# Optimization experiments

Hardware: AMD Instinct MI355X
Metric: run time of the kernel (lower is better)

## Reference

```python
import jax, jax.numpy as jnp
import numpy as np

N_BALLS, BALL, DIM, HEADS = 16, 512, 256, 8
DH = DIM // HEADS            # 32
WIN = BALL // 16             # sliding window = 32
CBS = BALL // 16             # compress block size = 32
CST = BALL // 32             # compress stride = 16
FBS = BALL // 16             # fine (selection) block size = 32
NCB = (BALL - CBS) // CST + 1  # 31 compressed blocks
NFB = BALL // FBS              # 16 fine blocks
NB = BALL // WIN               # 16 sliding blocks
SCALE = DH ** -0.5

# ---- static index maps / masks (numpy, baked at trace time) ----
_qi = np.arange(BALL)
WIDX = np.arange(NCB)[:, None] * CST + np.arange(CBS)[None, :]          # (NCB, CBS)
_blk_end = np.arange(NCB) * CST + CBS - 1
CMASK = np.concatenate([np.ones((BALL, 1), bool), _qi[:, None] >= _blk_end[None, :]], axis=1)  # (m, NCB+1), col0 = mem kv
OVERLAP = np.zeros((NCB, NFB), np.float32)  # fraction of compressed block j overlapping fine block f
for _j in range(NCB):
    _a, _b = _j * CST, _j * CST + CBS
    for _f in range(NFB):
        _fa, _fb = _f * FBS, (_f + 1) * FBS
        OVERLAP[_j, _f] = max(0, min(_b, _fb) - max(_a, _fa)) / CBS
SELMASK = np.arange(NFB)[None, :] < (_qi // FBS)[:, None]   # only strictly-past fine blocks selectable
HAS_SEL = (_qi // FBS) > 0
OWN_TRI = (_qi % FBS)[:, None] >= np.arange(FBS)[None, :]   # causal mask inside own fine block
_qq = np.arange(WIN)[None, :, None]
_kk = np.arange(2 * WIN)[None, None, :]
_bb = np.arange(NB)[:, None, None]
SWMASK = (_kk > _qq) & (_kk <= _qq + WIN) & ((_bb > 0) | (_kk >= WIN))
NEG = -jnp.inf


def _rot(x, tpos):
    # interleaved rotary over full head dim; x: (n,H,m,DH)
    d2 = DH // 2
    inv = 1.0 / (10000.0 ** (jnp.arange(d2, dtype=jnp.float32) / d2))
    ang = tpos[:, None] * inv[None, :]
    cos, sin = jnp.cos(ang), jnp.sin(ang)
    x1, x2 = x[..., 0::2], x[..., 1::2]
    return jnp.stack((x1 * cos - x2 * sin, x1 * sin + x2 * cos), axis=-1).reshape(x.shape)


def _gmlp(xw, w1, w2):
    # per-head grouped MLP compressing each window: (n,H,NCB,CBS,DH) -> (n,H,NCB,DH)
    f = xw.reshape(xw.shape[0], HEADS, NCB, CBS * DH)
    h = jax.nn.relu(jnp.einsum('nhbi,hio->nhbo', f, w1))
    return jnp.einsum('nhbi,hio->nhbo', h, w2)


def _forward(x, pos, Wpe, bpe, rms_w, Wqkv, kpos, vpos, kw1, kw2, vw1, vw2, mem_ck, mem_cv, Wg, Wo):
    n, m = N_BALLS, BALL
    # relative position embedding w.r.t. ball center (eq. 9)
    pb = pos.reshape(n, m, -1)
    rel = pb - pb.mean(axis=1, keepdims=True)
    hx = x.reshape(n, m, DIM) + rel @ Wpe + bpe
    # RMSNorm
    hn = hx * jax.lax.rsqrt(jnp.mean(hx * hx, axis=-1, keepdims=True) + 1e-6) * rms_w
    q, k, v = jnp.split(hn @ Wqkv, 3, axis=-1)
    heads = lambda t: t.reshape(n, m, HEADS, DH).transpose(0, 2, 1, 3)
    q, k, v = heads(q), heads(k), heads(v)
    tpos = jnp.arange(m, dtype=jnp.float32)
    rq, rk = _rot(q, tpos), _rot(k, tpos)

    # ---- compressed branch (non-rotated q/k, intra-block pos emb, 1 learned mem kv) ----
    kw = k[:, :, WIDX] + kpos[None, :, None]        # (n,H,NCB,CBS,DH)
    vw = v[:, :, WIDX] + vpos[None, :, None]
    ck = _gmlp(kw, kw1, kw2)
    cv = _gmlp(vw, vw1, vw2)
    ckf = jnp.concatenate([jnp.broadcast_to(mem_ck[None], (n, HEADS, 1, DH)), ck], axis=2)
    cvf = jnp.concatenate([jnp.broadcast_to(mem_cv[None], (n, HEADS, 1, DH)), cv], axis=2)
    csim = jnp.einsum('nhid,nhjd->nhij', q, ckf) * SCALE
    cattn = jax.nn.softmax(jnp.where(CMASK[None, None], csim, NEG), axis=-1)
    c_out = jnp.einsum('nhij,nhjd->nhid', cattn, cvf)

    # ---- fine selection: importance from compressed attn probs -> top-1 past fine block ----
    imp = jnp.einsum('nhij,jf->nhif', cattn[..., 1:], jnp.asarray(OVERLAP))  # (n,H,m,NFB)
    sel = jnp.argmax(jnp.where(SELMASK[None, None], imp, NEG), axis=-1)     # (n,H,m)
    kb = rk.reshape(n, HEADS, NFB, FBS, DH)
    vb = v.reshape(n, HEADS, NFB, FBS, DH)
    qb = rq.reshape(n, HEADS, NFB, FBS, DH)
    own_s = (jnp.einsum('nhfqd,nhfkd->nhfqk', qb, kb) * SCALE).reshape(n, HEADS, m, FBS)
    fk = jnp.take_along_axis(kb, sel[..., None, None], axis=2)  # (n,H,m,FBS,DH) gather
    fv = jnp.take_along_axis(vb, sel[..., None, None], axis=2)
    sel_s = jnp.einsum('nhid,nhikd->nhik', rq, fk) * SCALE
    scores = jnp.concatenate([jnp.where(OWN_TRI[None, None], own_s, NEG),
                              jnp.where(HAS_SEL[None, None, :, None], sel_s, NEG)], axis=-1)
    fattn = jax.nn.softmax(scores, axis=-1)
    f_out = (jnp.einsum('nhfqk,nhfkd->nhfqd', fattn[..., :FBS].reshape(n, HEADS, NFB, FBS, FBS), vb).reshape(n, HEADS, m, DH)
             + jnp.einsum('nhik,nhikd->nhid', fattn[..., FBS:], fv))

    # ---- sliding window branch (causal local attention, look-back 1 block) ----
    qw = rq.reshape(n, HEADS, NB, WIN, DH)
    kwb = rk.reshape(n, HEADS, NB, WIN, DH)
    vwb = v.reshape(n, HEADS, NB, WIN, DH)
    pad = ((0, 0), (0, 0), (1, 0), (0, 0), (0, 0))
    K2 = jnp.concatenate([jnp.pad(kwb, pad)[:, :, :NB], kwb], axis=3)
    V2 = jnp.concatenate([jnp.pad(vwb, pad)[:, :, :NB], vwb], axis=3)
    s_sw = jnp.einsum('nhbqd,nhbkd->nhbqk', qw, K2) * SCALE
    sattn = jax.nn.softmax(jnp.where(SWMASK[None, None], s_sw, NEG), axis=-1)
    sw_out = jnp.einsum('nhbqk,nhbkd->nhbqd', sattn, V2).reshape(n, HEADS, m, DH)

    # ---- sigmoid-gated combine of the 3 strategies, merge heads, out proj ----
    gates = jax.nn.sigmoid(hn @ Wg).reshape(n, m, HEADS, 3).transpose(0, 2, 1, 3)  # (n,H,m,3)
    o = c_out * gates[..., 0:1] + f_out * gates[..., 1:2] + sw_out * gates[..., 2:3]
    o = o.transpose(0, 2, 1, 3).reshape(n, m, DIM)
    return (o @ Wo).reshape(n * m, DIM)


def setup_inputs() -> dict:
    key = jax.random.key(0)
    ks = jax.random.split(key, 16)
    s = 0.02
    N = N_BALLS * BALL
    return dict(
        x=jax.random.normal(ks[0], (N, DIM), jnp.float32),
        pos=jax.random.normal(ks[1], (N, 3), jnp.float32),
        Wpe=s * jax.random.normal(ks[2], (3, DIM), jnp.float32),
        bpe=jnp.zeros((DIM,), jnp.float32),
        rms_w=jnp.ones((DIM,), jnp.float32),
        Wqkv=s * jax.random.normal(ks[3], (DIM, 3 * DIM), jnp.float32),
        kpos=s * jax.random.normal(ks[4], (HEADS, CBS, DH), jnp.float32),
        vpos=s * jax.random.normal(ks[5], (HEADS, CBS, DH), jnp.float32),
        kw1=s * jax.random.normal(ks[6], (HEADS, CBS * DH, CBS * DH), jnp.float32),
        kw2=s * jax.random.normal(ks[7], (HEADS, CBS * DH, DH), jnp.float32),
        vw1=s * jax.random.normal(ks[8], (HEADS, CBS * DH, CBS * DH), jnp.float32),
        vw2=s * jax.random.normal(ks[9], (HEADS, CBS * DH, DH), jnp.float32),
        mem_ck=s * jax.random.normal(ks[10], (HEADS, 1, DH), jnp.float32),
        mem_cv=s * jax.random.normal(ks[11], (HEADS, 1, DH), jnp.float32),
        Wg=s * jax.random.normal(ks[12], (DIM, 3 * HEADS), jnp.float32),
        Wo=s * jax.random.normal(ks[13], (DIM, DIM), jnp.float32),
    )


def reference(x, pos, Wpe, bpe, rms_w, Wqkv, kpos, vpos, kw1, kw2, vw1, vw2, mem_ck, mem_cv, Wg, Wo):
    return _forward(x, pos, Wpe, bpe, rms_w, Wqkv, kpos, vpos, kw1, kw2, vw1, vw2, mem_ck, mem_cv, Wg, Wo)
```

## Files before the change

### kernel.cpp

```cpp
#include <hip/hip_runtime.h>
#include <hip/hip_bf16.h>
#include <math.h>

#define SCALE_ 0.17677669529663687f

__global__ __launch_bounds__(256) void d_rope(float* __restrict__ rope) {
  int i = blockIdx.x * 256 + threadIdx.x;
  int t = i >> 4, j = i & 15;
  float inv = powf(10000.f, -(float)j / 16.f);
  float ang = (float)t * inv;
  rope[2 * i]     = cosf(ang);
  rope[2 * i + 1] = sinf(ang);
}

__global__ __launch_bounds__(256) void k_pm(const float* __restrict__ pos,
                                            float* __restrict__ pm) {
  __shared__ float ps[1536];
  int ball = blockIdx.x;
  for (int i = threadIdx.x; i < 1536; i += 256) ps[i] = pos[(size_t)ball * 1536 + i];
  __syncthreads();
  if (threadIdx.x < 3) {
    int c = threadIdx.x;
    float s = 0.f;
    for (int t = 0; t < 512; ++t) s += ps[t * 3 + c];
    pm[ball * 3 + c] = s * (1.f / 512.f);
  }
}

__global__ __launch_bounds__(256) void k_hn(const float* __restrict__ x,
                                            const float* __restrict__ pos,
                                            const float* __restrict__ pm,
                                            const float* __restrict__ Wpe,
                                            const float* __restrict__ bpe,
                                            const float* __restrict__ rmsw,
                                            const float* __restrict__ Wg,
                                            float* __restrict__ hn,
                                            float* __restrict__ gates) {
  __shared__ float hx[32][257];
  __shared__ float rr[32][3];
  __shared__ float invs[32];
  int tb = blockIdx.x * 32;
  if (threadIdx.x < 96) {
    int tok = threadIdx.x / 3, c = threadIdx.x % 3;
    rr[tok][c] = pos[(size_t)(tb + tok) * 3 + c] - pm[((tb + tok) >> 9) * 3 + c];
  }
  __syncthreads();
  for (int i = threadIdx.x; i < 8192; i += 256) {
    int tok = i >> 8, d = i & 255;
    float h = x[(size_t)(tb + tok) * 256 + d] + rr[tok][0] * Wpe[d] + rr[tok][1] * Wpe[256 + d]
            + rr[tok][2] * Wpe[512 + d] + bpe[d];
    hx[tok][d] = h;
  }
  __syncthreads();
  if (threadIdx.x < 32) {
    int tok = threadIdx.x;
    float ss = 0.f;
    for (int d = 0; d < 256; ++d) { float h = hx[tok][d]; ss += h * h; }
    invs[tok] = 1.f / sqrtf(ss * (1.f / 256.f) + 1e-6f);
  }
  __syncthreads();
  for (int i = threadIdx.x; i < 8192; i += 256) {
    int tok = i >> 8, d = i & 255;
    float hv = hx[tok][d] * invs[tok] * rmsw[d];
    hn[(size_t)(tb + tok) * 256 + d] = hv;
    hx[tok][d] = hv;
  }
  __syncthreads();
  for (int g = threadIdx.x; g < 768; g += 256) {
    int tok = g / 24, j = g % 24;
    float s = 0.f;
    for (int d = 0; d < 256; ++d) s += hx[tok][d] * Wg[d * 24 + j];
    gates[(size_t)(tb + tok) * 24 + j] = 1.f / (1.f + expf(-s));
  }
}

__global__ __launch_bounds__(256) void k_qkv(const float* __restrict__ A,
                                             const float* __restrict__ B,
                                             const float* __restrict__ rope,
                                             float* __restrict__ qo,
                                             float* __restrict__ ko,
                                             float* __restrict__ vo,
                                             float* __restrict__ rqo,
                                             float* __restrict__ rko) {
  __shared__ float As[32][66];
  __shared__ __align__(16) float Bs[32][68];
  const int bid = blockIdx.x;
  const int xcd = bid & 7;
  const int idx = bid >> 3;
  const int m0 = (xcd * 16 + (idx & 15)) * 64;
  const int n0 = (idx >> 4) * 64;
  const int tid = threadIdx.x;
  const int tx = tid & 15, ty = tid >> 4;
  float acc[4][4] = {};
  for (int k0 = 0; k0 < 256; k0 += 32) {
#pragma unroll
    for (int i = 0; i < 8; ++i) {
      int li = tid + i * 256;
      int mm = li >> 5, c = li & 31;
      As[c][mm] = A[(size_t)(m0 + mm) * 256 + k0 + c];
    }
#pragma unroll
    for (int i = 0; i < 8; ++i) {
      int li = tid + i * 256;
      int r = li >> 6, c = li & 63;
      Bs[r][c] = B[(size_t)(k0 + r) * 768 + n0 + c];
    }
    __syncthreads();
#pragma unroll
    for (int kk = 0; kk < 32; ++kk) {
      float2 a0 = *reinterpret_cast<const float2*>(&As[kk][ty * 4]);
      float2 a1 = *reinterpret_cast<const float2*>(&As[kk][ty * 4 + 2]);
      float4 b4 = *reinterpret_cast<const float4*>(&Bs[kk][tx * 4]);
      float a[4] = {a0.x, a0.y, a1.x, a1.y};
      float b[4] = {b4.x, b4.y, b4.z, b4.w};
#pragma unroll
      for (int i = 0; i < 4; ++i)
#pragma unroll
        for (int j = 0; j < 4; ++j) acc[i][j] += a[i] * b[j];
    }
    __syncthreads();
  }
#pragma unroll
  for (int i = 0; i < 4; ++i) {
    int row = m0 + ty * 4 + i;
    int nb = row >> 9, t = row & 511;
#pragma unroll
    for (int j = 0; j < 4; j += 2) {
      int col = n0 + tx * 4 + j;
      int which = col >> 8, cj = col & 255;
      int h = cj >> 5, d = cj & 31;
      float v1 = acc[i][j], v2 = acc[i][j + 1];
      size_t base = ((size_t)(nb * 8 + h) * 512 + t) * 32 + d;
      if (which == 0) {
        qo[base] = v1; qo[base + 1] = v2;
        int p = d >> 1;
        float cc = rope[(t * 16 + p) * 2], ss = rope[(t * 16 + p) * 2 + 1];
        rqo[base] = v1 * cc - v2 * ss; rqo[base + 1] = v1 * ss + v2 * cc;
      } else if (which == 1) {
        ko[base] = v1; ko[base + 1] = v2;
        int p = d >> 1;
        float cc = rope[(t * 16 + p) * 2], ss = rope[(t * 16 + p) * 2 + 1];
        rko[base] = v1 * cc - v2 * ss; rko[base + 1] = v1 * ss + v2 * cc;
      } else {
        vo[base] = v1; vo[base + 1] = v2;
      }
    }
  }
}

__global__ __launch_bounds__(256) void k_gmlp1(const float* __restrict__ kv,
                                               const float* __restrict__ posw,
                                               const float* __restrict__ w1,
                                               float* __restrict__ hb) {
  __shared__ float As[32][66];
  __shared__ __align__(16) float Bs[32][68];
  __shared__ int rowbase[64];
  const int bid = blockIdx.x;
  const int xcd = bid & 7;
  const int idx = bid >> 3;
  const int mt  = idx & 7;
  const int nh  = xcd * 16 + (idx >> 3);
  const int n0 = (nh & 15) * 64;
  const int h  = nh >> 4;
  const int m0 = mt * 64;
  const int tid = threadIdx.x;
  const int tx = tid & 15, ty = tid >> 4;
  if (tid < 64) {
    int row = m0 + tid;
    if (row < 496) {
      int nb = row / 31, bb = row % 31;
      rowbase[tid] = ((nb * 8 + h) * 512 + bb * 16) * 32;
    } else rowbase[tid] = -1;
  }
  __syncthreads();
  float acc[4][4] = {};
  const float* pw = posw + h * 1024;
  for (int k0 = 0; k0 < 1024; k0 += 32) {
#pragma unroll
    for (int i = 0; i < 8; ++i) {
      int li = tid + i * 256;
      int mm = li >> 5, c = li & 31;
      int base = rowbase[mm];
      float vv = 0.f;
      if (base >= 0) vv = kv[(size_t)base + k0 + c] + pw[k0 + c];
      As[c][mm] = vv;
    }
#pragma unroll
    for (int i = 0; i < 8; ++i) {
      int li = tid + i * 256;
      int r = li >> 6, c = li & 63;
      Bs[r][c] = w1[(size_t)h * 1048576 + (size_t)(k0 + r) * 1024 + n0 + c];
    }
    __syncthreads();
#pragma unroll
    for (int kk = 0; kk < 32; ++kk) {
      float2 a0 = *reinterpret_cast<const float2*>(&As[kk][ty * 4]);
      float2 a1 = *reinterpret_cast<const float2*>(&As[kk][ty * 4 + 2]);
      float4 b4 = *reinterpret_cast<const float4*>(&Bs[kk][tx * 4]);
      float a[4] = {a0.x, a0.y, a1.x, a1.y};
      float b[4] = {b4.x, b4.y, b4.z, b4.w};
#pragma unroll
      for (int i = 0; i < 4; ++i)
#pragma unroll
        for (int j = 0; j < 4; ++j) acc[i][j] += a[i] * b[j];
    }
    __syncthreads();
  }
#pragma unroll
  for (int i = 0; i < 4; ++i) {
    int row = m0 + ty * 4 + i;
    if (row < 496) {
#pragma unroll
      for (int j = 0; j < 4; ++j)
        hb[((size_t)h * 496 + row) * 1024 + n0 + tx * 4 + j] = fmaxf(acc[i][j], 0.f);
    }
  }
}

__global__ __launch_bounds__(256) void d_g2(const float* __restrict__ hh,
                                            const float* __restrict__ w2,
                                            float* __restrict__ outp) {
  int gid = blockIdx.x * 256 + threadIdx.x;
  int o = gid & 31;
  int rem = gid >> 5;
  int h = rem / 496, row = rem % 496;
  int nb = row / 31, bb = row % 31;
  const float* hr = hh + (size_t)rem * 1024;
  const float* w2p = w2 + (size_t)h * 32768 + o;
  float s = 0.f;
  for (int i = 0; i < 1024; ++i) s += hr[i] * w2p[(size_t)i * 32];
  outp[((size_t)(nb * 8 + h) * 31 + bb) * 32 + o] = s;
}

__global__ __launch_bounds__(256) void k_cattn(const float* __restrict__ q,
                                               const float* __restrict__ ck,
                                               const float* __restrict__ cv,
                                               const float* __restrict__ mem_ck,
                                               const float* __restrict__ mem_cv,
                                               const float* __restrict__ gates,
                                               float* __restrict__ obuf,
                                               int* __restrict__ sel) {
  int nh = blockIdx.x;
  int h = nh & 7, ball = nh >> 3;
  __shared__ float kf[32][33], vf[32][33];
  for (int i = threadIdx.x; i < 1024; i += 256) {
    int j = i >> 5, d = i & 31;
    kf[j][d] = (j == 0) ? mem_ck[h * 32 + d] : ck[((size_t)nh * 31 + j - 1) * 32 + d];
    vf[j][d] = (j == 0) ? mem_cv[h * 32 + d] : cv[((size_t)nh * 31 + j - 1) * 32 + d];
  }
  __syncthreads();
  for (int t = threadIdx.x; t < 512; t += 256) {
    const float* qp = q + ((size_t)nh * 512 + t) * 32;
    float qr[32];
#pragma unroll
    for (int d = 0; d < 32; ++d) qr[d] = qp[d];
    float sc[32];
    float mx = -INFINITY;
#pragma unroll
    for (int j = 0; j < 32; ++j) {
      float s = -INFINITY;
      bool valid = (j == 0) || (t >= (j - 1) * 16 + 31);
      if (valid) {
        s = 0.f;
        for (int d = 0; d < 32; ++d) s += qr[d] * kf[j][d];
        s *= SCALE_;
      }
      sc[j] = s;
      mx = fmaxf(mx, s);
    }
    float e[32];
    float den = 0.f;
#pragma unroll
    for (int j = 0; j < 32; ++j) { e[j] = expf(sc[j] - mx); den += e[j]; }
    float num[32];
#pragma unroll
    for (int d = 0; d < 32; ++d) num[d] = 0.f;
#pragma unroll
    for (int j = 0; j < 32; ++j) {
      float p = e[j];
      for (int d = 0; d < 32; ++d) num[d] += p * vf[j][d];
    }
    float inv = 1.f / den;
    float g0 = gates[(size_t)(ball * 512 + t) * 24 + h * 3];
    float* op = obuf + (size_t)(ball * 512 + t) * 256 + h * 32;
    for (int d = 0; d < 32; ++d) op[d] = num[d] * inv * g0;

    int s_idx = 0;
    if (t >= 32) {
      int fn = t >> 5;
      float best = -INFINITY;
      for (int f = 0; f < fn; ++f) {
        float im = 0.f;
#pragma unroll
        for (int j = 0; j < 31; ++j) {
          int a = j * 16, b2 = a + 32, fa = f * 32, fb = fa + 32;
          int lo = a > fa ? a : fa;
          int hi = b2 < fb ? b2 : fb;
          if (hi > lo) im += e[j + 1] * (float)(hi - lo) * (1.f / 32.f);
        }
        if (im > best) { best = im; s_idx = f; }
      }
    }
    sel[(size_t)nh * 512 + t] = s_idx;
  }
}

__global__ __launch_bounds__(256) void k_fattn(const float* __restrict__ rq,
                                               const float* __restrict__ rk,
                                               const float* __restrict__ v,
                                               const int* __restrict__ sel,
                                               const float* __restrict__ gates,
                                               float* __restrict__ obuf) {
  int f0 = blockIdx.x, h = blockIdx.y, nb = blockIdx.z;
  int nh = nb * 8 + h;
  __shared__ float rqs[32][33], rks[32][33], vs[32][33];
  for (int i = threadIdx.x; i < 1024; i += 256) {
    int r = i >> 5, d = i & 31;
    size_t base = ((size_t)nh * 512 + f0 * 32 + r) * 32 + d;
    rqs[r][d] = rq[base];
    rks[r][d] = rk[base];
    vs[r][d]  = v[base];
  }
  __syncthreads();
  int qi = threadIdx.x >> 3, l = threadIdx.x & 7;
  int t = f0 * 32 + qi;
  int sb = sel[(size_t)nh * 512 + t];
  bool hs = (t >= 32);
  float p[8];
  float mx = -INFINITY;
#pragma unroll
  for (int kk2 = 0; kk2 < 8; ++kk2) {
    int kk = l * 8 + kk2;
    float s = -INFINITY;
    if (kk < 32) {
      if (qi >= kk) {
        s = 0.f;
#pragma unroll
        for (int d = 0; d < 32; ++d) s += rqs[qi][d] * rks[kk][d];
        s *= SCALE_;
      }
    } else if (hs) {
      const float* kp = rk + ((size_t)nh * 512 + sb * 32 + (kk - 32)) * 32;
      s = 0.f;
#pragma unroll
      for (int d = 0; d < 32; ++d) s += rqs[qi][d] * kp[d];
      s *= SCALE_;
    }
    p[kk2] = s;
    mx = fmaxf(mx, s);
  }
#pragma unroll
  for (int off = 4; off; off >>= 1) mx = fmaxf(mx, __shfl_xor(mx, off, 8));
  float sum = 0.f;
#pragma unroll
  for (int kk2 = 0; kk2 < 8; ++kk2) { p[kk2] = expf(p[kk2] - mx); sum += p[kk2]; }
#pragma unroll
  for (int off = 4; off; off >>= 1) sum += __shfl_xor(sum, off, 8);
  float inv = 1.f / sum;
  float acc[32];
#pragma unroll
  for (int d = 0; d < 32; ++d) acc[d] = 0.f;
#pragma unroll
  for (int kk2 = 0; kk2 < 8; ++kk2) {
    int kk = l * 8 + kk2;
    float pw = p[kk2] * inv;
    if (kk < 32) {
#pragma unroll
      for (int d = 0; d < 32; ++d) acc[d] += pw * vs[kk][d];
    } else if (hs) {
      const float* vp = v + ((size_t)nh * 512 + sb * 32 + (kk - 32)) * 32;
#pragma unroll
      for (int d = 0; d < 32; ++d) acc[d] += pw * vp[d];
    }
  }
#pragma unroll
  for (int off = 4; off; off >>= 1) {
#pragma unroll
    for (int d = 0; d < 32; ++d) acc[d] += __shfl_xor(acc[d], off, 8);
  }
  float g1 = gates[(size_t)(nb * 512 + t) * 24 + h * 3 + 1];
  float* op = obuf + (size_t)(nb * 512 + t) * 256 + h * 32;
#pragma unroll
  for (int j = 0; j < 4; ++j) op[l * 4 + j] += acc[l * 4 + j] * g1;
}

__global__ __launch_bounds__(256) void k_swattn(const float* __restrict__ rq,
                                                const float* __restrict__ rk,
                                                const float* __restrict__ v,
                                                const float* __restrict__ gates,
                                                float* __restrict__ obuf) {
  int b = blockIdx.x, h = blockIdx.y, nb = blockIdx.z;
  int nh = nb * 8 + h;
  __shared__ float rqs[32][33], k2s[64][33], v2s[64][33];
  for (int i = threadIdx.x; i < 1024; i += 256) {
    int r = i >> 5, d = i & 31;
    rqs[r][d] = rq[((size_t)nh * 512 + b * 32 + r) * 32 + d];
  }
  for (int i = threadIdx.x; i < 2048; i += 256) {
    int r = i >> 5, d = i & 31;
    int tk = (b - 1) * 32 + r;
    float kk_ = 0.f, vv_ = 0.f;
    if (tk >= 0) {
      kk_ = rk[((size_t)nh * 512 + tk) * 32 + d];
      vv_ = v[((size_t)nh * 512 + tk) * 32 + d];
    }
    k2s[r][d] = kk_;
    v2s[r][d] = vv_;
  }
  __syncthreads();
  int qi = threadIdx.x >> 3, l = threadIdx.x & 7;
  int t = b * 32 + qi;
  float p[8];
  float mx = -INFINITY;
#pragma unroll
  for (int kk2 = 0; kk2 < 8; ++kk2) {
    int kk = l * 8 + kk2;
    bool valid = (kk > qi) && (kk <= qi + 32) && ((b > 0) || (kk >= 32));
    float s = -INFINITY;
    if (valid) {
      s = 0.f;
#pragma unroll
      for (int d = 0; d < 32; ++d) s += rqs[qi][d] * k2s[kk][d];
      s *= SCALE_;
    }
    p[kk2] = s;
    mx = fmaxf(mx, s);
  }
#pragma unroll
  for (int off = 4; off; off >>= 1) mx = fmaxf(mx, __shfl_xor(mx, off, 8));
  float sum = 0.f;
#pragma unroll
  for (int kk2 = 0; kk2 < 8; ++kk2) { p[kk2] = expf(p[kk2] - mx); sum += p[kk2]; }
#pragma unroll
  for (int off = 4; off; off >>= 1) sum += __shfl_xor(sum, off, 8);
  float inv = 1.f / sum;
  float acc[32];
#pragma unroll
  for (int d = 0; d < 32; ++d) acc[d] = 0.f;
#pragma unroll
  for (int kk2 = 0; kk2 < 8; ++kk2) {
    int kk = l * 8 + kk2;
    float pw = p[kk2] * inv;
#pragma unroll
    for (int d = 0; d < 32; ++d) acc[d] += pw * v2s[kk][d];
  }
#pragma unroll
  for (int off = 4; off; off >>= 1) {
#pragma unroll
    for (int d = 0; d < 32; ++d) acc[d] += __shfl_xor(acc[d], off, 8);
  }
  float g2 = gates[(size_t)(nb * 512 + t) * 24 + h * 3 + 2];
  float* op = obuf + (size_t)(nb * 512 + t) * 256 + h * 32;
#pragma unroll
  for (int j = 0; j < 4; ++j) op[l * 4 + j] += acc[l * 4 + j] * g2;
}

__global__ __launch_bounds__(256) void k_out(const float* __restrict__ A,
                                             const float* __restrict__ B,
                                             float* __restrict__ C) {
  __shared__ float As[32][66];
  __shared__ __align__(16) float Bs[32][68];
  const int bid = blockIdx.x;
  const int xcd = bid & 7;
  const int idx = bid >> 3;
  const int m0 = (xcd * 16 + (idx & 15)) * 64;
  const int n0 = (idx >> 4) * 64;
  const int tid = threadIdx.x;
  const int tx = tid & 15, ty = tid >> 4;
  float acc[4][4] = {};
  for (int k0 = 0; k0 < 256; k0 += 32) {
#pragma unroll
    for (int i = 0; i < 8; ++i) {
      int li = tid + i * 256;
      int mm = li >> 5, c = li & 31;
      As[c][mm] = A[(size_t)(m0 + mm) * 256 + k0 + c];
    }
#pragma unroll
    for (int i = 0; i < 8; ++i) {
      int li = tid + i * 256;
      int r = li >> 6, c = li & 63;
      Bs[r][c] = B[(size_t)(k0 + r) * 256 + n0 + c];
    }
    __syncthreads();
#pragma unroll
    for (int kk = 0; kk < 32; ++kk) {
      float2 a0 = *reinterpret_cast<const float2*>(&As[kk][ty * 4]);
      float2 a1 = *reinterpret_cast<const float2*>(&As[kk][ty * 4 + 2]);
      float4 b4 = *reinterpret_cast<const float4*>(&Bs[kk][tx * 4]);
      float a[4] = {a0.x, a0.y, a1.x, a1.y};
      float b[4] = {b4.x, b4.y, b4.z, b4.w};
#pragma unroll
      for (int i = 0; i < 4; ++i)
#pragma unroll
        for (int j = 0; j < 4; ++j) acc[i][j] += a[i] * b[j];
    }
    __syncthreads();
  }
#pragma unroll
  for (int i = 0; i < 4; ++i) {
    int row = m0 + ty * 4 + i;
#pragma unroll
    for (int j = 0; j < 4; ++j)
      C[(size_t)row * 256 + n0 + tx * 4 + j] = acc[i][j];
  }
}

extern "C" void kernel_launch(void* const* d_in, const int* in_sizes, int n_in,
                              void* d_out, int out_size, void* d_ws, size_t ws_size,
                              hipStream_t stream) {
  const float* x      = (const float*)d_in[0];
  const float* pos    = (const float*)d_in[1];
  const float* Wpe    = (const float*)d_in[2];
  const float* bpe    = (const float*)d_in[3];
  const float* rms_w  = (const float*)d_in[4];
  const float* Wqkv   = (const float*)d_in[5];
  const float* kpos   = (const float*)d_in[6];
  const float* vpos   = (const float*)d_in[7];
  const float* kw1    = (const float*)d_in[8];
  const float* kw2    = (const float*)d_in[9];
  const float* vw1    = (const float*)d_in[10];
  const float* vw2    = (const float*)d_in[11];
  const float* mem_ck = (const float*)d_in[12];
  const float* mem_cv = (const float*)d_in[13];
  const float* Wg     = (const float*)d_in[14];
  const float* Wo     = (const float*)d_in[15];
  float* out = (float*)d_out;

  float* ws = (float*)d_ws;
  const size_t TOK = 2097152;
  float* hn    = ws;
  float* q     = ws + TOK;
  float* k     = ws + 2 * TOK;
  float* v     = ws + 3 * TOK;
  float* rq    = ws + 4 * TOK;
  float* rk    = ws + 5 * TOK;
  float* obuf  = ws + 6 * TOK;
  float* hh    = ws + 7 * TOK;
  float* ck    = hh + 4063232;
  float* cv    = ck + 126976;
  float* gates = cv + 126976;
  float* rope  = gates + 196608;
  float* pm    = rope + 16384;
  int*   sel   = (int*)(pm + 64);

  d_rope<<<32, 256, 0, stream>>>(rope);
  k_pm<<<16, 256, 0, stream>>>(pos, pm);
  k_hn<<<256, 256, 0, stream>>>(x, pos, pm, Wpe, bpe, rms_w, Wg, hn, gates);
  k_qkv<<<1536, 256, 0, stream>>>(hn, Wqkv, rope, q, k, v, rq, rk);
  k_gmlp1<<<1024, 256, 0, stream>>>(k, kpos, kw1, hh);
  d_g2<<<496, 256, 0, stream>>>(hh, kw2, ck);
  k_gmlp1<<<1024, 256, 0, stream>>>(v, vpos, vw1, hh);
  d_g2<<<496, 256, 0, stream>>>(hh, vw2, cv);
  k_cattn<<<128, 256, 0, stream>>>(q, ck, cv, mem_ck, mem_cv, gates, obuf, sel);
  k_fattn<<<dim3(16, 8, 16), 256, 0, stream>>>(rq, rk, v, sel, gates, obuf);
  k_swattn<<<dim3(16, 8, 16), 256, 0, stream>>>(rq, rk, v, gates, obuf);
  k_out<<<512, 256, 0, stream>>>(obuf, Wo, out);
}
```

Before: 620.4 us.

## Fuse fine and sliding attention, vectorize GEMM tile loads, split cattn blocks

Merges the rope and position-mean kernels into one launch, and fuses the fine-selection and sliding-window attention kernels so shared tiles are loaded once and obuf gets a single read-modify-write. GEMM tile loads in the qkv, gmlp1 and output kernels now use float4 global reads, and gmlp1 drops its shared rowbase table by computing row offsets inline. The compressed-attention kernel is split over twice as many blocks, one token per thread, to raise parallelism. The fused attention kernel keeps both attention paths' registers live, which may raise register pressure.

```diff
diff --git a/kernel.cpp b/kernel.cpp
--- a/kernel.cpp
+++ b/kernel.cpp
@@ -4,26 +4,27 @@
 
 #define SCALE_ 0.17677669529663687f
 
-__global__ __launch_bounds__(256) void d_rope(float* __restrict__ rope) {
-  int i = blockIdx.x * 256 + threadIdx.x;
-  int t = i >> 4, j = i & 15;
-  float inv = powf(10000.f, -(float)j / 16.f);
-  float ang = (float)t * inv;
-  rope[2 * i]     = cosf(ang);
-  rope[2 * i + 1] = sinf(ang);
-}
-
-__global__ __launch_bounds__(256) void k_pm(const float* __restrict__ pos,
-                                            float* __restrict__ pm) {
+__global__ __launch_bounds__(256) void k_pre(const float* __restrict__ pos,
+                                             float* __restrict__ rope,
+                                             float* __restrict__ pm) {
   __shared__ float ps[1536];
-  int ball = blockIdx.x;
-  for (int i = threadIdx.x; i < 1536; i += 256) ps[i] = pos[(size_t)ball * 1536 + i];
-  __syncthreads();
-  if (threadIdx.x < 3) {
-    int c = threadIdx.x;
-    float s = 0.f;
-    for (int t = 0; t < 512; ++t) s += ps[t * 3 + c];
-    pm[ball * 3 + c] = s * (1.f / 512.f);
+  if (blockIdx.x < 32) {
+    int i = blockIdx.x * 256 + threadIdx.x;
+    int t = i >> 4, j = i & 15;
+    float inv = powf(10000.f, -(float)j / 16.f);
+    float ang = (float)t * inv;
+    rope[2 * i]     = cosf(ang);
+    rope[2 * i + 1] = sinf(ang);
+  } else {
+    int ball = blockIdx.x - 32;
+    for (int i = threadIdx.x; i < 1536; i += 256) ps[i] = pos[(size_t)ball * 1536 + i];
+    __syncthreads();
+    if (threadIdx.x < 3) {
+      int c = threadIdx.x;
+      float s = 0.f;
+      for (int t = 0; t < 512; ++t) s += ps[t * 3 + c];
+      pm[ball * 3 + c] = s * (1.f / 512.f);
+    }
   }
 }
 
@@ -94,16 +95,19 @@
   float acc[4][4] = {};
   for (int k0 = 0; k0 < 256; k0 += 32) {
 #pragma unroll
-    for (int i = 0; i < 8; ++i) {
+    for (int i = 0; i < 2; ++i) {
       int li = tid + i * 256;
-      int mm = li >> 5, c = li & 31;
-      As[c][mm] = A[(size_t)(m0 + mm) * 256 + k0 + c];
-    }
-#pragma unroll
-    for (int i = 0; i < 8; ++i) {
+      int mm = li >> 3, c4 = li & 7;
+      float4 a4 = *reinterpret_cast<const float4*>(&A[(size_t)(m0 + mm) * 256 + k0 + c4 * 4]);
+      As[c4 * 4 + 0][mm] = a4.x; As[c4 * 4 + 1][mm] = a4.y;
+      As[c4 * 4 + 2][mm] = a4.z; As[c4 * 4 + 3][mm] = a4.w;
+    }
+#pragma unroll
+    for (int i = 0; i < 2; ++i) {
       int li = tid + i * 256;
-      int r = li >> 6, c = li & 63;
-      Bs[r][c] = B[(size_t)(k0 + r) * 768 + n0 + c];
+      int r = li >> 4, c4 = li & 15;
+      float4 b4 = *reinterpret_cast<const float4*>(&B[(size_t)(k0 + r) * 768 + n0 + c4 * 4]);
+      *reinterpret_cast<float4*>(&Bs[r][c4 * 4]) = b4;
     }
     __syncthreads();
 #pragma unroll
@@ -154,7 +158,6 @@
                                                float* __restrict__ hb) {
   __shared__ float As[32][66];
   __shared__ __align__(16) float Bs[32][68];
-  __shared__ int rowbase[64];
   const int bid = blockIdx.x;
   const int xcd = bid & 7;
   const int idx = bid >> 3;
@@ -165,31 +168,32 @@
   const int m0 = mt * 64;
   const int tid = threadIdx.x;
   const int tx = tid & 15, ty = tid >> 4;
-  if (tid < 64) {
-    int row = m0 + tid;
-    if (row < 496) {
-      int nb = row / 31, bb = row % 31;
-      rowbase[tid] = ((nb * 8 + h) * 512 + bb * 16) * 32;
-    } else rowbase[tid] = -1;
-  }
-  __syncthreads();
+  const float* pw = posw + h * 1024;
   float acc[4][4] = {};
-  const float* pw = posw + h * 1024;
   for (int k0 = 0; k0 < 1024; k0 += 32) {
 #pragma unroll
-    for (int i = 0; i < 8; ++i) {
+    for (int i = 0; i < 2; ++i) {
       int li = tid + i * 256;
-      int mm = li >> 5, c = li & 31;
-      int base = rowbase[mm];
-      float vv = 0.f;
-      if (base >= 0) vv = kv[(size_t)base + k0 + c] + pw[k0 + c];
-      As[c][mm] = vv;
-    }
-#pragma unroll
-    for (int i = 0; i < 8; ++i) {
+      int mm = li >> 3, c4 = li & 7;
+      int row = m0 + mm;
+      float4 av = {0.f, 0.f, 0.f, 0.f};
+      if (row < 496) {
+        int nb = row / 31, bb = row % 31;
+        float4 k4 = *reinterpret_cast<const float4*>(
+            &kv[((size_t)(nb * 8 + h) * 512 + bb * 16) * 32 + k0 + c4 * 4]);
+        float4 p4 = *reinterpret_cast<const float4*>(&pw[k0 + c4 * 4]);
+        av.x = k4.x + p4.x; av.y = k4.y + p4.y; av.z = k4.z + p4.z; av.w = k4.w + p4.w;
+      }
+      As[c4 * 4 + 0][mm] = av.x; As[c4 * 4 + 1][mm] = av.y;
+      As[c4 * 4 + 2][mm] = av.z; As[c4 * 4 + 3][mm] = av.w;
+    }
+#pragma unroll
+    for (int i = 0; i < 2; ++i) {
       int li = tid + i * 256;
-      int r = li >> 6, c = li & 63;
-      Bs[r][c] = w1[(size_t)h * 1048576 + (size_t)(k0 + r) * 1024 + n0 + c];
+      int r = li >> 4, c4 = li & 15;
+      float4 b4 = *reinterpret_cast<const float4*>(
+          &w1[(size_t)h * 1048576 + (size_t)(k0 + r) * 1024 + n0 + c4 * 4]);
+      *reinterpret_cast<float4*>(&Bs[r][c4 * 4]) = b4;
     }
     __syncthreads();
 #pragma unroll
@@ -240,8 +244,9 @@
                                                const float* __restrict__ gates,
                                                float* __restrict__ obuf,
                                                int* __restrict__ sel) {
-  int nh = blockIdx.x;
+  int nh = blockIdx.x >> 1;
   int h = nh & 7, ball = nh >> 3;
+  int t = (blockIdx.x & 1) * 256 + threadIdx.x;
   __shared__ float kf[32][33], vf[32][33];
   for (int i = threadIdx.x; i < 1024; i += 256) {
     int j = i >> 5, d = i & 31;
@@ -249,146 +254,66 @@
     vf[j][d] = (j == 0) ? mem_cv[h * 32 + d] : cv[((size_t)nh * 31 + j - 1) * 32 + d];
   }
   __syncthreads();
-  for (int t = threadIdx.x; t < 512; t += 256) {
-    const float* qp = q + ((size_t)nh * 512 + t) * 32;
-    float qr[32];
-#pragma unroll
-    for (int d = 0; d < 32; ++d) qr[d] = qp[d];
-    float sc[32];
-    float mx = -INFINITY;
-#pragma unroll
-    for (int j = 0; j < 32; ++j) {
-      float s = -INFINITY;
-      bool valid = (j == 0) || (t >= (j - 1) * 16 + 31);
-      if (valid) {
-        s = 0.f;
-        for (int d = 0; d < 32; ++d) s += qr[d] * kf[j][d];
-        s *= SCALE_;
+  const float* qp = q + ((size_t)nh * 512 + t) * 32;
+  float qr[32];
+#pragma unroll
+  for (int d = 0; d < 32; ++d) qr[d] = qp[d];
+  float sc[32];
+  float mx = -INFINITY;
+#pragma unroll
+  for (int j = 0; j < 32; ++j) {
+    float s = -INFINITY;
+    bool valid = (j == 0) || (t >= (j - 1) * 16 + 31);
+    if (valid) {
+      s = 0.f;
+      for (int d = 0; d < 32; ++d) s += qr[d] * kf[j][d];
+      s *= SCALE_;
+    }
+    sc[j] = s;
+    mx = fmaxf(mx, s);
+  }
+  float e[32];
+  float den = 0.f;
+#pragma unroll
+  for (int j = 0; j < 32; ++j) { e[j] = expf(sc[j] - mx); den += e[j]; }
+  float num[32];
+#pragma unroll
+  for (int d = 0; d < 32; ++d) num[d] = 0.f;
+#pragma unroll
+  for (int j = 0; j < 32; ++j) {
+    float p = e[j];
+    for (int d = 0; d < 32; ++d) num[d] += p * vf[j][d];
+  }
+  float inv = 1.f / den;
+  float g0 = gates[(size_t)(ball * 512 + t) * 24 + h * 3];
+  float* op = obuf + (size_t)(ball * 512 + t) * 256 + h * 32;
+  for (int d = 0; d < 32; ++d) op[d] = num[d] * inv * g0;
+
+  int s_idx = 0;
+  if (t >= 32) {
+    int fn = t >> 5;
+    float best = -INFINITY;
+    for (int f = 0; f < fn; ++f) {
+      float im = 0.f;
+#pragma unroll
+      for (int j = 0; j < 31; ++j) {
+        int a = j * 16, b2 = a + 32, fa = f * 32, fb = fa + 32;
+        int lo = a > fa ? a : fa;
+        int hi = b2 < fb ? b2 : fb;
+        if (hi > lo) im += e[j + 1] * (float)(hi - lo) * (1.f / 32.f);
       }
-      sc[j] = s;
-      mx = fmaxf(mx, s);
-    }
-    float e[32];
-    float den = 0.f;
-#pragma unroll
-    for (int j = 0; j < 32; ++j) { e[j] = expf(sc[j] - mx); den += e[j]; }
-    float num[32];
-#pragma unroll
-    for (int d = 0; d < 32; ++d) num[d] = 0.f;
-#pragma unroll
-    for (int j = 0; j < 32; ++j) {
-      float p = e[j];
-      for (int d = 0; d < 32; ++d) num[d] += p * vf[j][d];
-    }
-    float inv = 1.f / den;
-    float g0 = gates[(size_t)(ball * 512 + t) * 24 + h * 3];
-    float* op = obuf + (size_t)(ball * 512 + t) * 256 + h * 32;
-    for (int d = 0; d < 32; ++d) op[d] = num[d] * inv * g0;
-
-    int s_idx = 0;
-    if (t >= 32) {
-      int fn = t >> 5;
-      float best = -INFINITY;
-      for (int f = 0; f < fn; ++f) {
-        float im = 0.f;
-#pragma unroll
-        for (int j = 0; j < 31; ++j) {
-          int a = j * 16, b2 = a + 32, fa = f * 32, fb = fa + 32;
-          int lo = a > fa ? a : fa;
-          int hi = b2 < fb ? b2 : fb;
-          if (hi > lo) im += e[j + 1] * (float)(hi - lo) * (1.f / 32.f);
-        }
-        if (im > best) { best = im; s_idx = f; }
-      }
-    }
-    sel[(size_t)nh * 512 + t] = s_idx;
-  }
-}
-
-__global__ __launch_bounds__(256) void k_fattn(const float* __restrict__ rq,
-                                               const float* __restrict__ rk,
-                                               const float* __restrict__ v,
-                                               const int* __restrict__ sel,
-                                               const float* __restrict__ gates,
-                                               float* __restrict__ obuf) {
-  int f0 = blockIdx.x, h = blockIdx.y, nb = blockIdx.z;
-  int nh = nb * 8 + h;
-  __shared__ float rqs[32][33], rks[32][33], vs[32][33];
-  for (int i = threadIdx.x; i < 1024; i += 256) {
-    int r = i >> 5, d = i & 31;
-    size_t base = ((size_t)nh * 512 + f0 * 32 + r) * 32 + d;
-    rqs[r][d] = rq[base];
-    rks[r][d] = rk[base];
-    vs[r][d]  = v[base];
-  }
-  __syncthreads();
-  int qi = threadIdx.x >> 3, l = threadIdx.x & 7;
-  int t = f0 * 32 + qi;
-  int sb = sel[(size_t)nh * 512 + t];
-  bool hs = (t >= 32);
-  float p[8];
-  float mx = -INFINITY;
-#pragma unroll
-  for (int kk2 = 0; kk2 < 8; ++kk2) {
-    int kk = l * 8 + kk2;
-    float s = -INFINITY;
-    if (kk < 32) {
-      if (qi >= kk) {
-        s = 0.f;
-#pragma unroll
-        for (int d = 0; d < 32; ++d) s += rqs[qi][d] * rks[kk][d];
-        s *= SCALE_;
-      }
-    } else if (hs) {
-      const float* kp = rk + ((size_t)nh * 512 + sb * 32 + (kk - 32)) * 32;
-      s = 0.f;
-#pragma unroll
-      for (int d = 0; d < 32; ++d) s += rqs[qi][d] * kp[d];
-      s *= SCALE_;
-    }
-    p[kk2] = s;
-    mx = fmaxf(mx, s);
-  }
-#pragma unroll
-  for (int off = 4; off; off >>= 1) mx = fmaxf(mx, __shfl_xor(mx, off, 8));
-  float sum = 0.f;
-#pragma unroll
-  for (int kk2 = 0; kk2 < 8; ++kk2) { p[kk2] = expf(p[kk2] - mx); sum += p[kk2]; }
-#pragma unroll
-  for (int off = 4; off; off >>= 1) sum += __shfl_xor(sum, off, 8);
-  float inv = 1.f / sum;
-  float acc[32];
-#pragma unroll
-  for (int d = 0; d < 32; ++d) acc[d] = 0.f;
-#pragma unroll
-  for (int kk2 = 0; kk2 < 8; ++kk2) {
-    int kk = l * 8 + kk2;
-    float pw = p[kk2] * inv;
-    if (kk < 32) {
-#pragma unroll
-      for (int d = 0; d < 32; ++d) acc[d] += pw * vs[kk][d];
-    } else if (hs) {
-      const float* vp = v + ((size_t)nh * 512 + sb * 32 + (kk - 32)) * 32;
-#pragma unroll
-      for (int d = 0; d < 32; ++d) acc[d] += pw * vp[d];
-    }
-  }
-#pragma unroll
-  for (int off = 4; off; off >>= 1) {
-#pragma unroll
-    for (int d = 0; d < 32; ++d) acc[d] += __shfl_xor(acc[d], off, 8);
-  }
-  float g1 = gates[(size_t)(nb * 512 + t) * 24 + h * 3 + 1];
-  float* op = obuf + (size_t)(nb * 512 + t) * 256 + h * 32;
-#pragma unroll
-  for (int j = 0; j < 4; ++j) op[l * 4 + j] += acc[l * 4 + j] * g1;
-}
-
-__global__ __launch_bounds__(256) void k_swattn(const float* __restrict__ rq,
-                                                const float* __restrict__ rk,
-                                                const float* __restrict__ v,
-                                                const float* __restrict__ gates,
-                                                float* __restrict__ obuf) {
+      if (im > best) { best = im; s_idx = f; }
+    }
+  }
+  sel[(size_t)nh * 512 + t] = s_idx;
+}
+
+__global__ __launch_bounds__(256) void k_fsw(const float* __restrict__ rq,
+                                             const float* __restrict__ rk,
+                                             const float* __restrict__ v,
+                                             const int* __restrict__ sel,
+                                             const float* __restrict__ gates,
+                                             float* __restrict__ obuf) {
   int b = blockIdx.x, h = blockIdx.y, nb = blockIdx.z;
   int nh = nb * 8 + h;
   __shared__ float rqs[32][33], k2s[64][33], v2s[64][33];
@@ -410,49 +335,122 @@
   __syncthreads();
   int qi = threadIdx.x >> 3, l = threadIdx.x & 7;
   int t = b * 32 + qi;
-  float p[8];
-  float mx = -INFINITY;
-#pragma unroll
-  for (int kk2 = 0; kk2 < 8; ++kk2) {
-    int kk = l * 8 + kk2;
-    bool valid = (kk > qi) && (kk <= qi + 32) && ((b > 0) || (kk >= 32));
-    float s = -INFINITY;
-    if (valid) {
-      s = 0.f;
-#pragma unroll
-      for (int d = 0; d < 32; ++d) s += rqs[qi][d] * k2s[kk][d];
-      s *= SCALE_;
-    }
-    p[kk2] = s;
-    mx = fmaxf(mx, s);
-  }
-#pragma unroll
-  for (int off = 4; off; off >>= 1) mx = fmaxf(mx, __shfl_xor(mx, off, 8));
-  float sum = 0.f;
-#pragma unroll
-  for (int kk2 = 0; kk2 < 8; ++kk2) { p[kk2] = expf(p[kk2] - mx); sum += p[kk2]; }
-#pragma unroll
-  for (int off = 4; off; off >>= 1) sum += __shfl_xor(sum, off, 8);
-  float inv = 1.f / sum;
-  float acc[32];
-#pragma unroll
-  for (int d = 0; d < 32; ++d) acc[d] = 0.f;
-#pragma unroll
-  for (int kk2 = 0; kk2 < 8; ++kk2) {
-    int kk = l * 8 + kk2;
-    float pw = p[kk2] * inv;
-#pragma unroll
-    for (int d = 0; d < 32; ++d) acc[d] += pw * v2s[kk][d];
-  }
-#pragma unroll
-  for (int off = 4; off; off >>= 1) {
-#pragma unroll
-    for (int d = 0; d < 32; ++d) acc[d] += __shfl_xor(acc[d], off, 8);
-  }
+
+  int sb = sel[(size_t)nh * 512 + t];
+  bool hs = (t >= 32);
+  float fo[4];
+  {
+    float p[8];
+    float mx = -INFINITY;
+#pragma unroll
+    for (int kk2 = 0; kk2 < 8; ++kk2) {
+      int kk = l * 8 + kk2;
+      float s = -INFINITY;
+      if (kk < 32) {
+        if (qi >= kk) {
+          s = 0.f;
+#pragma unroll
+          for (int d = 0; d < 32; ++d) s += rqs[qi][d] * k2s[32 + kk][d];
+          s *= SCALE_;
+        }
+      } else if (hs) {
+        const float* kp = rk + ((size_t)nh * 512 + sb * 32 + (kk - 32)) * 32;
+        s = 0.f;
+#pragma unroll
+        for (int d = 0; d < 32; ++d) s += rqs[qi][d] * kp[d];
+        s *= SCALE_;
+      }
+      p[kk2] = s;
+      mx = fmaxf(mx, s);
+    }
+#pragma unroll
+    for (int off = 4; off; off >>= 1) mx = fmaxf(mx, __shfl_xor(mx, off, 8));
+    float sum = 0.f;
+#pragma unroll
+    for (int kk2 = 0; kk2 < 8; ++kk2) { p[kk2] = expf(p[kk2] - mx); sum += p[kk2]; }
+#pragma unroll
+    for (int off = 4; off; off >>= 1) sum += __shfl_xor(sum, off, 8);
+    float inv = 1.f / sum;
+    float acc[32];
+#pragma unroll
+    for (int d = 0; d < 32; ++d) acc[d] = 0.f;
+#pragma unroll
+    for (int kk2 = 0; kk2 < 8; ++kk2) {
+      int kk = l * 8 + kk2;
+      float pwt = p[kk2] * inv;
+      if (kk < 32) {
+#pragma unroll
+        for (int d = 0; d < 32; ++d) acc[d] += pwt * v2s[32 + kk][d];
+      } else if (hs) {
+        const float* vp = v + ((size_t)nh * 512 + sb * 32 + (kk - 32)) * 32;
+#pragma unroll
+        for (int d = 0; d < 32; ++d) acc[d] += pwt * vp[d];
+      }
+    }
+#pragma unroll
+    for (int off = 4; off; off >>= 1) {
+#pragma unroll
+      for (int d = 0; d < 32; ++d) acc[d] += __shfl_xor(acc[d], off, 8);
+    }
+#pragma unroll
+    for (int j = 0; j < 4; ++j) fo[j] = acc[l * 4 + j];
+  }
+
+  float so[4];
+  {
+    float p[8];
+    float mx = -INFINITY;
+#pragma unroll
+    for (int kk2 = 0; kk2 < 8; ++kk2) {
+      int kk = l * 8 + kk2;
+      bool valid = (kk > qi) && (kk <= qi + 32) && ((b > 0) || (kk >= 32));
+      float s = -INFINITY;
+      if (valid) {
+        s = 0.f;
+#pragma unroll
+        for (int d = 0; d < 32; ++d) s += rqs[qi][d] * k2s[kk][d];
+        s *= SCALE_;
+      }
+      p[kk2] = s;
+      mx = fmaxf(mx, s);
+    }
+#pragma unroll
+    for (int off = 4; off; off >>= 1) mx = fmaxf(mx, __shfl_xor(mx, off, 8));
+    float sum = 0.f;
+#pragma unroll
+    for (int kk2 = 0; kk2 < 8; ++kk2) { p[kk2] = expf(p[kk2] - mx); sum += p[kk2]; }
+#pragma unroll
+    for (int off = 4; off; off >>= 1) sum += __shfl_xor(sum, off, 8);
+    float inv = 1.f / sum;
+    float acc[32];
+#pragma unroll
+    for (int d = 0; d < 32; ++d) acc[d] = 0.f;
+#pragma unroll
+    for (int kk2 = 0; kk2 < 8; ++kk2) {
+      int kk = l * 8 + kk2;
+      float pwt = p[kk2] * inv;
+#pragma unroll
+      for (int d = 0; d < 32; ++d) acc[d] += pwt * v2s[kk][d];
+    }
+#pragma unroll
+    for (int off = 4; off; off >>= 1) {
+#pragma unroll
+      for (int d = 0; d < 32; ++d) acc[d] += __shfl_xor(acc[d], off, 8);
+    }
+#pragma unroll
+    for (int j = 0; j < 4; ++j) so[j] = acc[l * 4 + j];
+  }
+
+  float g1 = gates[(size_t)(nb * 512 + t) * 24 + h * 3 + 1];
   float g2 = gates[(size_t)(nb * 512 + t) * 24 + h * 3 + 2];
   float* op = obuf + (size_t)(nb * 512 + t) * 256 + h * 32;
 #pragma unroll
-  for (int j = 0; j < 4; ++j) op[l * 4 + j] += acc[l * 4 + j] * g2;
+  for (int j = 0; j < 4; ++j) {
+    float cur = op[l * 4 + j];
+    cur += fo[j] * g1;
+    cur += so[j] * g2;
+    op[l * 4 + j] = cur;
+  }
 }
 
 __global__ __launch_bounds__(256) void k_out(const float* __restrict__ A,
@@ -470,16 +468,19 @@
   float acc[4][4] = {};
   for (int k0 = 0; k0 < 256; k0 += 32) {
 #pragma unroll
-    for (int i = 0; i < 8; ++i) {
+    for (int i = 0; i < 2; ++i) {
       int li = tid + i * 256;
-      int mm = li >> 5, c = li & 31;
-      As[c][mm] = A[(size_t)(m0 + mm) * 256 + k0 + c];
-    }
-#pragma unroll
-    for (int i = 0; i < 8; ++i) {
+      int mm = li >> 3, c4 = li & 7;
+      float4 a4 = *reinterpret_cast<const float4*>(&A[(size_t)(m0 + mm) * 256 + k0 + c4 * 4]);
+      As[c4 * 4 + 0][mm] = a4.x; As[c4 * 4 + 1][mm] = a4.y;
+      As[c4 * 4 + 2][mm] = a4.z; As[c4 * 4 + 3][mm] = a4.w;
+    }
+#pragma unroll
+    for (int i = 0; i < 2; ++i) {
       int li = tid + i * 256;
-      int r = li >> 6, c = li & 63;
-      Bs[r][c] = B[(size_t)(k0 + r) * 256 + n0 + c];
+      int r = li >> 4, c4 = li & 15;
+      float4 b4 = *reinterpret_cast<const float4*>(&B[(size_t)(k0 + r) * 256 + n0 + c4 * 4]);
+      *reinterpret_cast<float4*>(&Bs[r][c4 * 4]) = b4;
     }
     __syncthreads();
 #pragma unroll
@@ -543,16 +544,14 @@
   float* pm    = rope + 16384;
   int*   sel   = (int*)(pm + 64);
 
-  d_rope<<<32, 256, 0, stream>>>(rope);
-  k_pm<<<16, 256, 0, stream>>>(pos, pm);
+  k_pre<<<48, 256, 0, stream>>>(pos, rope, pm);
   k_hn<<<256, 256, 0, stream>>>(x, pos, pm, Wpe, bpe, rms_w, Wg, hn, gates);
   k_qkv<<<1536, 256, 0, stream>>>(hn, Wqkv, rope, q, k, v, rq, rk);
   k_gmlp1<<<1024, 256, 0, stream>>>(k, kpos, kw1, hh);
   d_g2<<<496, 256, 0, stream>>>(hh, kw2, ck);
   k_gmlp1<<<1024, 256, 0, stream>>>(v, vpos, vw1, hh);
   d_g2<<<496, 256, 0, stream>>>(hh, vw2, cv);
-  k_cattn<<<128, 256, 0, stream>>>(q, ck, cv, mem_ck, mem_cv, gates, obuf, sel);
-  k_fattn<<<dim3(16, 8, 16), 256, 0, stream>>>(rq, rk, v, sel, gates, obuf);
-  k_swattn<<<dim3(16, 8, 16), 256, 0, stream>>>(rq, rk, v, gates, obuf);
+  k_cattn<<<256, 256, 0, stream>>>(q, ck, cv, mem_ck, mem_cv, gates, obuf, sel);
+  k_fsw<<<dim3(16, 8, 16), 256, 0, stream>>>(rq, rk, v, sel, gates, obuf);
   k_out<<<512, 256, 0, stream>>>(obuf, Wo, out);
 }
```

Result: faster. 561.9 us (-9.4%).
